# Kernel optimization log

Hardware: AMD Instinct MI355X
Metric: run time of the kernel (lower is better)

## Reference

```python
import jax, jax.numpy as jnp
import numpy as np

B, N, D_MODEL, H = 2, 2048, 1024, 16
Q_CHUNK, K_CHUNK = 512, 1024
LN_EPS = 1e-5


def layer_norm(x, g, b):
    mu = x.mean(-1, keepdims=True)
    var = ((x - mu) ** 2).mean(-1, keepdims=True)
    return (x - mu) * jax.lax.rsqrt(var + LN_EPS) * g + b


def chunked_attention(q, k, v, qry_chunk, key_chunk):
    # q,k,v: [b,h,n,d]; memory-efficient chunked online-softmax attention
    b, h, n, d = q.shape
    q = q * (d ** -0.5)
    Q, K = n // qry_chunk, n // key_chunk
    qr = q.reshape(b, h, Q, qry_chunk, d)
    kr = k.reshape(b, h, K, key_chunk, d)
    vr = v.reshape(b, h, K, key_chunk, d)
    # per (q-chunk, k-chunk) scores: [b,h,Q,K,i,j]
    qk = jnp.einsum('bhqid,bhkjd->bhqkij', qr, kr)
    qk_max = jax.lax.stop_gradient(qk.max(axis=-1, keepdims=True))  # [b,h,Q,K,i,1]
    exp_qk = jnp.exp(qk - qk_max)
    attn = jnp.einsum('bhqkij,bhkjd->bhqkid', exp_qk, vr)
    exp_sum = exp_qk.sum(-1)            # [b,h,Q,K,i]
    m = qk_max[..., 0]                  # [b,h,Q,K,i]
    gmax = m.max(axis=3, keepdims=True)  # global max over key chunks
    renorm = jax.lax.stop_gradient(jnp.exp(m - gmax))
    num = (attn * renorm[..., None]).sum(axis=3)       # [b,h,Q,i,d]
    den = (exp_sum * renorm).sum(axis=3)[..., None]    # [b,h,Q,i,1]
    out = num / (1e-8 + den)
    return out.reshape(b, h, n, d)


def setup_inputs() -> dict:
    key = jax.random.key(0)
    ks = jax.random.split(key, 10)
    s = 0.02
    return {
        'x': jax.random.normal(ks[0], (B, N, D_MODEL), dtype=jnp.float32),
        'Wq': jax.random.normal(ks[1], (D_MODEL, D_MODEL), dtype=jnp.float32) * s,
        'bq': jnp.zeros((D_MODEL,), jnp.float32),
        'Wk': jax.random.normal(ks[2], (D_MODEL, D_MODEL), dtype=jnp.float32) * s,
        'bk': jnp.zeros((D_MODEL,), jnp.float32),
        'Wv': jax.random.normal(ks[3], (D_MODEL, D_MODEL), dtype=jnp.float32) * s,
        'bv': jnp.zeros((D_MODEL,), jnp.float32),
        'Wo': jax.random.normal(ks[4], (D_MODEL, D_MODEL), dtype=jnp.float32) * s,
        'bo': jnp.zeros((D_MODEL,), jnp.float32),
        'ln_g': jnp.ones((D_MODEL,), jnp.float32),
        'ln_b': jnp.zeros((D_MODEL,), jnp.float32),
    }


def reference(x, Wq, bq, Wk, bk, Wv, bv, Wo, bo, ln_g, ln_b):
    # qkv adapter: self-attention (key = val = qry = x)
    q = x @ Wq + bq
    k = x @ Wk + bk
    v = x @ Wv + bv
    # pre-norm on query path
    q = layer_norm(q, ln_g, ln_b)
    b, n, _ = q.shape
    d = D_MODEL // H
    qh = q.reshape(b, n, H, d).transpose(0, 2, 1, 3)
    kh = k.reshape(b, n, H, d).transpose(0, 2, 1, 3)
    vh = v.reshape(b, n, H, d).transpose(0, 2, 1, 3)
    attn = chunked_attention(qh, kh, vh, Q_CHUNK, K_CHUNK)
    out = attn.transpose(0, 2, 1, 3).reshape(b, n, D_MODEL)
    out = out + q  # residual with normed projected query
    return out @ Wo + bo
```

## Files before the change

kernel.cpp:

```cpp
#include <hip/hip_runtime.h>


typedef unsigned short u16;
typedef __attribute__((ext_vector_type(8))) short bf8v;
typedef __attribute__((ext_vector_type(4))) float f4v;

typedef __attribute__((address_space(1))) void gvoid;
typedef __attribute__((address_space(3))) void lvoid;
__device__ __forceinline__ void cp16(const void* g, void* l) {
  __builtin_amdgcn_global_load_lds((gvoid*)g, (lvoid*)l, 16, 0, 0);
}

__device__ __forceinline__ float bf2f(u16 u) {
  unsigned int x = ((unsigned int)u) << 16;
  float f; __builtin_memcpy(&f, &x, 4); return f;
}
__device__ __forceinline__ u16 f2bf(float f) {
  unsigned int x; __builtin_memcpy(&x, &f, 4);
  unsigned int r = (x + 0x7fffu + ((x >> 16) & 1u)) >> 16;
  return (u16)r;
}
__device__ __forceinline__ unsigned pack2bf(float a, float b) {
  unsigned ua, ub;
  __builtin_memcpy(&ua, &a, 4); __builtin_memcpy(&ub, &b, 4);
  return __builtin_amdgcn_perm(ub, ua, 0x07060302u);
}

#define KSCALE 0.18033688011f

__global__ void k_classify(const u16* a0, const u16* a1, const u16* a2, const u16* a3,
                           const u16* a4, const u16* a5, const u16* a6, const u16* a7,
                           const u16* a8, const u16* a9, const u16* a10, int* flags) {
  int t = threadIdx.x;
  if (t >= 11) return;
  const u16* arr[11] = {a0,a1,a2,a3,a4,a5,a6,a7,a8,a9,a10};
  const u16* p = arr[t];
  int ze = 0, no = 0, pe = 0;
  for (int i = 0; i < 128; ++i) {
    u16 he = p[2*i], ho = p[2*i+1];
    if (he == 0) ze++;
    if (ho != 0) no++;
    int e = (he >> 7) & 0xff;
    if (he == 0 || (e >= 64 && e <= 160)) pe++;
  }
  int isbf;
  if (ze >= 100 && no >= 64) isbf = 0;
  else isbf = (pe >= 100) ? 1 : 0;
  flags[t] = isbf;
}

__global__ __launch_bounds__(256) void k_convert_x(const void* xin, u16* xb, const int* flags) {
  size_t i = ((size_t)blockIdx.x * 256 + threadIdx.x) * 8;
  if (flags[0]) {
    *(float4*)(xb + i) = *((const float4*)((const u16*)xin + i));
  } else {
    const float* xf = (const float*)xin;
    float4 a = *(const float4*)(xf + i);
    float4 b = *(const float4*)(xf + i + 4);
    ushort4 o0, o1;
    o0.x = f2bf(a.x); o0.y = f2bf(a.y); o0.z = f2bf(a.z); o0.w = f2bf(a.w);
    o1.x = f2bf(b.x); o1.y = f2bf(b.y); o1.z = f2bf(b.z); o1.w = f2bf(b.w);
    *(ushort4*)(xb + i) = o0; *(ushort4*)(xb + i + 4) = o1;
  }
}

__global__ __launch_bounds__(256) void k_transpose_w(const void* W0, const void* W1,
    const void* W2, const void* W3, u16* wt, const int* flags) {
  __shared__ u16 tile[64 * 65];
  int z = blockIdx.z;
  const void* W = (z == 0) ? W0 : (z == 1) ? W1 : (z == 2) ? W2 : W3;
  int isb = flags[1 + 2*z];
  u16* dst = wt + (size_t)z * (1u << 20);
  int r0 = blockIdx.y * 64, c0 = blockIdx.x * 64;
  int t = threadIdx.x;
  for (int rr = 0; rr < 2; ++rr) {
    int row = rr * 32 + (t >> 3);
    int c8 = (t & 7) * 8;
    u16 v[8];
    if (isb) {
      const u16* Ws = (const u16*)W;
      ushort4 a = *(const ushort4*)&Ws[(size_t)(r0 + row) * 1024 + c0 + c8];
      ushort4 b = *(const ushort4*)&Ws[(size_t)(r0 + row) * 1024 + c0 + c8 + 4];
      v[0]=a.x; v[1]=a.y; v[2]=a.z; v[3]=a.w; v[4]=b.x; v[5]=b.y; v[6]=b.z; v[7]=b.w;
    } else {
      const float* Wf = (const float*)W;
      float4 a = *(const float4*)&Wf[(size_t)(r0 + row) * 1024 + c0 + c8];
      float4 b = *(const float4*)&Wf[(size_t)(r0 + row) * 1024 + c0 + c8 + 4];
      v[0]=f2bf(a.x); v[1]=f2bf(a.y); v[2]=f2bf(a.z); v[3]=f2bf(a.w);
      v[4]=f2bf(b.x); v[5]=f2bf(b.y); v[6]=f2bf(b.z); v[7]=f2bf(b.w);
    }
#pragma unroll
    for (int j = 0; j < 8; ++j) tile[row * 65 + c8 + j] = v[j];
  }
  __syncthreads();
  for (int rr = 0; rr < 2; ++rr) {
    int nrow = rr * 32 + (t >> 3);
    int k8 = (t & 7) * 8;
    u16 v[8];
#pragma unroll
    for (int j = 0; j < 8; ++j) v[j] = tile[(k8 + j) * 65 + nrow];
    ushort4 o0, o1;
    o0.x=v[0]; o0.y=v[1]; o0.z=v[2]; o0.w=v[3];
    o1.x=v[4]; o1.y=v[5]; o1.z=v[6]; o1.w=v[7];
    *(ushort4*)&dst[(size_t)(c0 + nrow) * 1024 + r0 + k8] = o0;
    *(ushort4*)&dst[(size_t)(c0 + nrow) * 1024 + r0 + k8 + 4] = o1;
  }
}

template <int MT>
__device__ __forceinline__ void gemm_bt(const u16* __restrict__ A, const u16* __restrict__ Bt,
    const void* __restrict__ bias, int bias_bf, void* __restrict__ Cout, int mode,
    float cscale) {
  constexpr int MI = MT / 32;
  __shared__ __align__(16) u16 As[2][MT * 32];
  __shared__ __align__(16) u16 Bs[2][128 * 32];
  const int tid = threadIdx.x;
  const int wave = tid >> 6, lane = tid & 63;
  const int qd = lane >> 4, ln = lane & 15;
  const int m0 = blockIdx.y * MT, n0 = blockIdx.x * 128;
  const int wr = (wave >> 1) * (MT / 2), wc = (wave & 1) * 64;
  const int r0 = wave * 16 + (lane >> 2);
  const int csrc = ((lane & 3) ^ ((lane >> 2) & 3)) * 8;
  const u16* Ag = &A[(size_t)m0 * 1024];
  const u16* Bg = &Bt[(size_t)n0 * 1024];
  const int co = (qd ^ (ln & 3)) * 8;
  f4v acc[MI][4];
#pragma unroll
  for (int i = 0; i < MI; ++i)
#pragma unroll
    for (int j = 0; j < 4; ++j) acc[i][j] = (f4v){0.f, 0.f, 0.f, 0.f};

#pragma unroll
  for (int t = 0; t < MT / 64; ++t)
    cp16(&Ag[(size_t)(t * 64 + r0) * 1024 + csrc], &As[0][(t * 256 + wave * 64) * 8]);
#pragma unroll
  for (int t = 0; t < 2; ++t)
    cp16(&Bg[(size_t)(t * 64 + r0) * 1024 + csrc], &Bs[0][(t * 256 + wave * 64) * 8]);

  for (int it = 0; it < 32; ++it) {
    __syncthreads();
    if (it < 31) {
      int ko = (it + 1) * 32;
      int bi = (it + 1) & 1;
#pragma unroll
      for (int t = 0; t < MT / 64; ++t)
        cp16(&Ag[(size_t)(t * 64 + r0) * 1024 + ko + csrc], &As[bi][(t * 256 + wave * 64) * 8]);
#pragma unroll
      for (int t = 0; t < 2; ++t)
        cp16(&Bg[(size_t)(t * 64 + r0) * 1024 + ko + csrc], &Bs[bi][(t * 256 + wave * 64) * 8]);
    }
    const u16* as = As[it & 1];
    const u16* bs = Bs[it & 1];
    bf8v af[MI], bfr[4];
#pragma unroll
    for (int i = 0; i < MI; ++i) af[i]  = *(const bf8v*)&as[(wr + i * 16 + ln) * 32 + co];
#pragma unroll
    for (int j = 0; j < 4; ++j) bfr[j] = *(const bf8v*)&bs[(wc + j * 16 + ln) * 32 + co];
#pragma unroll
    for (int i = 0; i < MI; ++i)
#pragma unroll
      for (int j = 0; j < 4; ++j)
        acc[i][j] = __builtin_amdgcn_mfma_f32_16x16x32_bf16(af[i], bfr[j], acc[i][j], 0, 0, 0);
  }
#pragma unroll
  for (int j = 0; j < 4; ++j) {
    int col = n0 + wc + j * 16 + ln;
    float bv = bias_bf ? bf2f(((const u16*)bias)[col]) : ((const float*)bias)[col];
#pragma unroll
    for (int i = 0; i < MI; ++i) {
      int row = m0 + wr + i * 16 + qd * 4;
      if (mode == 2) {
        ushort4 o4;
        o4.x = f2bf((acc[i][j][0] + bv) * cscale);
        o4.y = f2bf((acc[i][j][1] + bv) * cscale);
        o4.z = f2bf((acc[i][j][2] + bv) * cscale);
        o4.w = f2bf((acc[i][j][3] + bv) * cscale);
        int b_ = row >> 11, nl = row & 2047;
        int h_ = col >> 6, d6 = col & 63;
        int kt = nl >> 6, b0 = nl & 63;
        int c = b0 >> 5, g = (b0 >> 4) & 1, qd_f = (b0 >> 2) & 3;
        int dt = d6 >> 4, ln_f = d6 & 15;
        size_t off = (size_t)(b_ * 16 + h_) * 131072
                   + (size_t)(kt * 4096 + (c * 4 + dt) * 512 + (qd_f * 16 + ln_f) * 8 + g * 4);
        *(ushort4*)&((u16*)Cout)[off] = o4;
      } else {
#pragma unroll
        for (int r = 0; r < 4; ++r) {
          float v = (acc[i][j][r] + bv) * cscale;
          if (mode == 1) ((u16*)Cout)[(size_t)(row + r) * 1024 + col] = f2bf(v);
          else           ((float*)Cout)[(size_t)(row + r) * 1024 + col] = v;
        }
      }
    }
  }
}

__global__ __launch_bounds__(256) void k_gemm_qkv(const u16* xb, const u16* wt,
    const void* bq, const void* bk, const void* bv, const int* flags,
    u16* qpre, u16* kb, u16* vtb) {
  int z = blockIdx.z;
  const u16* Bt = wt + (size_t)z * (1u << 20);
  const void* bias = (z == 0) ? bq : (z == 1) ? bk : bv;
  if (z == 0)      gemm_bt<128>(xb, Bt, bias, flags[2], qpre, 1, 1.0f);
  else if (z == 1) gemm_bt<128>(xb, Bt, bias, flags[4], kb,   1, KSCALE);
  else             gemm_bt<128>(xb, Bt, bias, flags[6], vtb,  2, 1.0f);
}

__global__ __launch_bounds__(256) void k_gemm_out(const u16* A, const u16* Bt,
    const void* bias, const int* flags, void* out) {
  gemm_bt<64>(A, Bt, bias, flags[8], out, flags[0] ? 1 : 0, 1.0f);
}

__global__ __launch_bounds__(256) void k_layernorm(const u16* __restrict__ qp,
    const void* __restrict__ g, const void* __restrict__ bb, const int* flags,
    u16* __restrict__ out) {
  int row = blockIdx.x, t = threadIdx.x;
  const u16* rp = qp + (size_t)row * 1024;
  ushort4 u = *(const ushort4*)(rp + t * 4);
  float x0 = bf2f(u.x), x1 = bf2f(u.y), x2 = bf2f(u.z), x3 = bf2f(u.w);
  float s = x0 + x1 + x2 + x3;
  float s2 = x0 * x0 + x1 * x1 + x2 * x2 + x3 * x3;
  for (int off = 32; off; off >>= 1) { s += __shfl_down(s, off); s2 += __shfl_down(s2, off); }
  __shared__ float red[10];
  int wave = t >> 6, lane = t & 63;
  if (lane == 0) { red[wave] = s; red[4 + wave] = s2; }
  __syncthreads();
  if (t == 0) {
    float S = red[0] + red[1] + red[2] + red[3];
    float S2 = red[4] + red[5] + red[6] + red[7];
    float mu = S * (1.f / 1024.f);
    float var = S2 * (1.f / 1024.f) - mu * mu;
    red[8] = mu; red[9] = rsqrtf(var + 1e-5f);
  }
  __syncthreads();
  float mu = red[8], rstd = red[9];
  int gf = flags[9], bf = flags[10];
  int c = t * 4;
  float gv[4], bv[4];
#pragma unroll
  for (int k = 0; k < 4; ++k) {
    gv[k] = gf ? bf2f(((const u16*)g)[c + k]) : ((const float*)g)[c + k];
    bv[k] = bf ? bf2f(((const u16*)bb)[c + k]) : ((const float*)bb)[c + k];
  }
  ushort4 o;
  o.x = f2bf((x0 - mu) * rstd * gv[0] + bv[0]);
  o.y = f2bf((x1 - mu) * rstd * gv[1] + bv[1]);
  o.z = f2bf((x2 - mu) * rstd * gv[2] + bv[2]);
  o.w = f2bf((x3 - mu) * rstd * gv[3] + bv[3]);
  *(ushort4*)(out + (size_t)row * 1024 + c) = o;
}

__global__ __launch_bounds__(256) void k_attention(const u16* __restrict__ qln,
    const u16* __restrict__ kb, const u16* __restrict__ vfg, u16* __restrict__ attn) {
  const int x = blockIdx.x;
  const int xcd = x & 7, sl = x >> 3;
  const int bh = xcd * 4 + (sl >> 3), qc = sl & 7;
  const int b = bh >> 4, h = bh & 15;
  const int tid = threadIdx.x, wave = tid >> 6, lane = tid & 63;
  const int qd = lane >> 4, ln = lane & 15;
  const int qrow0 = qc * 256 + wave * 64;

  const u16* kgb = kb + (size_t)b * 2048 * 1024 + h * 64;
  const u16* vgb = vfg + (size_t)bh * 131072;

  bf8v qf[4][2];
#pragma unroll
  for (int qs = 0; qs < 4; ++qs) {
    const u16* qb = qln + ((size_t)b * 2048 + qrow0 + qs * 16 + ln) * 1024 + h * 64;
    qf[qs][0] = *(const bf8v*)(qb + qd * 8);
    qf[qs][1] = *(const bf8v*)(qb + 32 + qd * 8);
  }
  float ls[4][4];
  f4v o[4][4];
#pragma unroll
  for (int qs = 0; qs < 4; ++qs)
#pragma unroll
    for (int r = 0; r < 4; ++r) { ls[qs][r] = 0.f; o[qs][r] = (f4v){0.f, 0.f, 0.f, 0.f}; }

  for (int kt = 0; kt < 2048; kt += 64) {
    const u16* kr = kgb + (size_t)kt * 1024;
    bf8v kf[4][2];
#pragma unroll
    for (int ct = 0; ct < 4; ++ct) {
      kf[ct][0] = *(const bf8v*)(kr + (size_t)(ct * 16 + ln) * 1024 + qd * 8);
      kf[ct][1] = *(const bf8v*)(kr + (size_t)(ct * 16 + ln) * 1024 + 32 + qd * 8);
    }
    const u16* vr = vgb + (size_t)(kt >> 6) * 4096;
    bf8v vf[8];
#pragma unroll
    for (int cd = 0; cd < 8; ++cd)
      vf[cd] = *(const bf8v*)(vr + cd * 512 + lane * 8);

#pragma unroll
    for (int qs = 0; qs < 4; ++qs) {
      unsigned pk[4][2];
#pragma unroll
      for (int ct = 0; ct < 4; ++ct) {
        f4v z = (f4v){0.f, 0.f, 0.f, 0.f};
        z = __builtin_amdgcn_mfma_f32_16x16x32_bf16(kf[ct][0], qf[qs][0], z, 0, 0, 0);
        z = __builtin_amdgcn_mfma_f32_16x16x32_bf16(kf[ct][1], qf[qs][1], z, 0, 0, 0);
        float p0 = __builtin_amdgcn_exp2f(z[0]);
        float p1 = __builtin_amdgcn_exp2f(z[1]);
        float p2 = __builtin_amdgcn_exp2f(z[2]);
        float p3 = __builtin_amdgcn_exp2f(z[3]);
        ls[qs][0] += p0; ls[qs][1] += p1; ls[qs][2] += p2; ls[qs][3] += p3;
        pk[ct][0] = pack2bf(p0, p1);
        pk[ct][1] = pack2bf(p2, p3);
      }
#pragma unroll
      for (int c = 0; c < 2; ++c) {
        unsigned avals[4] = {pk[2*c][0], pk[2*c][1], pk[2*c+1][0], pk[2*c+1][1]};
        bf8v af; __builtin_memcpy(&af, avals, 16);
#pragma unroll
        for (int dt = 0; dt < 4; ++dt)
          o[qs][dt] = __builtin_amdgcn_mfma_f32_16x16x32_bf16(af, vf[c * 4 + dt], o[qs][dt], 0, 0, 0);
      }
    }
  }
#pragma unroll
  for (int qs = 0; qs < 4; ++qs) {
    float lsum = (ls[qs][0] + ls[qs][1]) + (ls[qs][2] + ls[qs][3]);
    lsum += __shfl_xor(lsum, 16);
    lsum += __shfl_xor(lsum, 32);
    float rden[4];
#pragma unroll
    for (int r = 0; r < 4; ++r) {
      float dv = __shfl(lsum, (lane & 48) + qd * 4 + r);
      rden[r] = __builtin_amdgcn_rcpf(1e-8f + dv);
    }
#pragma unroll
    for (int dt = 0; dt < 4; ++dt) {
#pragma unroll
      for (int r = 0; r < 4; ++r) {
        size_t idx = ((size_t)b * 2048 + qrow0 + qs * 16 + qd * 4 + r) * 1024
                   + h * 64 + dt * 16 + ln;
        float val = o[qs][dt][r] * rden[r] + bf2f(qln[idx]);
        attn[idx] = f2bf(val);
      }
    }
  }
}

extern "C" void kernel_launch(void* const* d_in, const int* in_sizes, int n_in,
                              void* d_out, int out_size, void* d_ws, size_t ws_size,
                              hipStream_t stream) {
  int* flags = (int*)d_ws;
  u16* base = (u16*)((char*)d_ws + 256);
  const size_t M1 = 1u << 20;
  u16* xb   = base;
  u16* wt   = base + 4 * M1;
  u16* qpre = base + 8 * M1;
  u16* kb   = base + 12 * M1;
  u16* vtb  = base + 16 * M1;
  u16* qln = xb;
  u16* at  = qpre;

  k_classify<<<1, 64, 0, stream>>>(
      (const u16*)d_in[0], (const u16*)d_in[1], (const u16*)d_in[2], (const u16*)d_in[3],
      (const u16*)d_in[4], (const u16*)d_in[5], (const u16*)d_in[6], (const u16*)d_in[7],
      (const u16*)d_in[8], (const u16*)d_in[9], (const u16*)d_in[10], flags);

  k_convert_x<<<2048, 256, 0, stream>>>(d_in[0], xb, flags);
  k_transpose_w<<<dim3(16, 16, 4), 256, 0, stream>>>(d_in[1], d_in[3], d_in[5], d_in[7], wt, flags);
  k_gemm_qkv<<<dim3(8, 32, 3), 256, 0, stream>>>(xb, wt, d_in[2], d_in[4], d_in[6], flags,
                                                 qpre, kb, vtb);
  k_layernorm<<<4096, 256, 0, stream>>>(qpre, d_in[9], d_in[10], flags, qln);
  k_attention<<<256, 256, 0, stream>>>(qln, kb, vtb, at);
  k_gemm_out<<<dim3(8, 64), 256, 0, stream>>>(at, wt + 3 * M1, d_in[8], flags, d_out);
}
```

Before: 228.0 us.

## Double-buffer K loads in attention, fuse prep kernels, parallelize classify

The attention loop now uses two K fragment register buffers, so the next tile's K loads are issued before the current tile's MFMAs, letting global-load latency overlap compute. The x conversion and the weight transposes are merged into one launch to save a kernel launch and fill the GPU better. The dtype classifier now uses one wavefront per input with a shuffle reduction instead of a serial loop per thread. These changes add register pressure in attention, which could lower occupancy.

```diff
diff --git a/kernel.cpp b/kernel.cpp
--- a/kernel.cpp
+++ b/kernel.cpp
@@ -31,79 +31,87 @@
 __global__ void k_classify(const u16* a0, const u16* a1, const u16* a2, const u16* a3,
                            const u16* a4, const u16* a5, const u16* a6, const u16* a7,
                            const u16* a8, const u16* a9, const u16* a10, int* flags) {
-  int t = threadIdx.x;
-  if (t >= 11) return;
+  int w = threadIdx.x >> 6, lane = threadIdx.x & 63;
+  if (w >= 11) return;
   const u16* arr[11] = {a0,a1,a2,a3,a4,a5,a6,a7,a8,a9,a10};
-  const u16* p = arr[t];
+  const u16* p = arr[w];
   int ze = 0, no = 0, pe = 0;
-  for (int i = 0; i < 128; ++i) {
+#pragma unroll
+  for (int rep = 0; rep < 2; ++rep) {
+    int i = rep * 64 + lane;
     u16 he = p[2*i], ho = p[2*i+1];
-    if (he == 0) ze++;
-    if (ho != 0) no++;
+    ze += (he == 0);
+    no += (ho != 0);
     int e = (he >> 7) & 0xff;
-    if (he == 0 || (e >= 64 && e <= 160)) pe++;
-  }
-  int isbf;
-  if (ze >= 100 && no >= 64) isbf = 0;
-  else isbf = (pe >= 100) ? 1 : 0;
-  flags[t] = isbf;
-}
-
-__global__ __launch_bounds__(256) void k_convert_x(const void* xin, u16* xb, const int* flags) {
-  size_t i = ((size_t)blockIdx.x * 256 + threadIdx.x) * 8;
-  if (flags[0]) {
-    *(float4*)(xb + i) = *((const float4*)((const u16*)xin + i));
+    pe += (he == 0 || (e >= 64 && e <= 160));
+  }
+  for (int off = 32; off; off >>= 1) {
+    ze += __shfl_down(ze, off); no += __shfl_down(no, off); pe += __shfl_down(pe, off);
+  }
+  if (lane == 0) {
+    int isbf;
+    if (ze >= 100 && no >= 64) isbf = 0;
+    else isbf = (pe >= 100) ? 1 : 0;
+    flags[w] = isbf;
+  }
+}
+
+__global__ __launch_bounds__(256) void k_prep(const void* xin, const void* W0,
+    const void* W1, const void* W2, const void* W3, u16* xb, u16* wt, const int* flags) {
+  __shared__ u16 tile[64 * 65];
+  int bx = blockIdx.x;
+  if (bx < 1024) {
+    int z = bx >> 8, t8 = bx & 255;
+    const void* W = (z == 0) ? W0 : (z == 1) ? W1 : (z == 2) ? W2 : W3;
+    int isb = flags[1 + 2*z];
+    u16* dst = wt + (size_t)z * (1u << 20);
+    int r0 = (t8 >> 4) * 64, c0 = (t8 & 15) * 64;
+    int t = threadIdx.x;
+    for (int rr = 0; rr < 2; ++rr) {
+      int row = rr * 32 + (t >> 3);
+      int c8 = (t & 7) * 8;
+      u16 v[8];
+      if (isb) {
+        const u16* Ws = (const u16*)W;
+        ushort4 a = *(const ushort4*)&Ws[(size_t)(r0 + row) * 1024 + c0 + c8];
+        ushort4 b = *(const ushort4*)&Ws[(size_t)(r0 + row) * 1024 + c0 + c8 + 4];
+        v[0]=a.x; v[1]=a.y; v[2]=a.z; v[3]=a.w; v[4]=b.x; v[5]=b.y; v[6]=b.z; v[7]=b.w;
+      } else {
+        const float* Wf = (const float*)W;
+        float4 a = *(const float4*)&Wf[(size_t)(r0 + row) * 1024 + c0 + c8];
+        float4 b = *(const float4*)&Wf[(size_t)(r0 + row) * 1024 + c0 + c8 + 4];
+        v[0]=f2bf(a.x); v[1]=f2bf(a.y); v[2]=f2bf(a.z); v[3]=f2bf(a.w);
+        v[4]=f2bf(b.x); v[5]=f2bf(b.y); v[6]=f2bf(b.z); v[7]=f2bf(b.w);
+      }
+#pragma unroll
+      for (int j = 0; j < 8; ++j) tile[row * 65 + c8 + j] = v[j];
+    }
+    __syncthreads();
+    for (int rr = 0; rr < 2; ++rr) {
+      int nrow = rr * 32 + (t >> 3);
+      int k8 = (t & 7) * 8;
+      u16 v[8];
+#pragma unroll
+      for (int j = 0; j < 8; ++j) v[j] = tile[(k8 + j) * 65 + nrow];
+      ushort4 o0, o1;
+      o0.x=v[0]; o0.y=v[1]; o0.z=v[2]; o0.w=v[3];
+      o1.x=v[4]; o1.y=v[5]; o1.z=v[6]; o1.w=v[7];
+      *(ushort4*)&dst[(size_t)(c0 + nrow) * 1024 + r0 + k8] = o0;
+      *(ushort4*)&dst[(size_t)(c0 + nrow) * 1024 + r0 + k8 + 4] = o1;
+    }
   } else {
-    const float* xf = (const float*)xin;
-    float4 a = *(const float4*)(xf + i);
-    float4 b = *(const float4*)(xf + i + 4);
-    ushort4 o0, o1;
-    o0.x = f2bf(a.x); o0.y = f2bf(a.y); o0.z = f2bf(a.z); o0.w = f2bf(a.w);
-    o1.x = f2bf(b.x); o1.y = f2bf(b.y); o1.z = f2bf(b.z); o1.w = f2bf(b.w);
-    *(ushort4*)(xb + i) = o0; *(ushort4*)(xb + i + 4) = o1;
-  }
-}
-
-__global__ __launch_bounds__(256) void k_transpose_w(const void* W0, const void* W1,
-    const void* W2, const void* W3, u16* wt, const int* flags) {
-  __shared__ u16 tile[64 * 65];
-  int z = blockIdx.z;
-  const void* W = (z == 0) ? W0 : (z == 1) ? W1 : (z == 2) ? W2 : W3;
-  int isb = flags[1 + 2*z];
-  u16* dst = wt + (size_t)z * (1u << 20);
-  int r0 = blockIdx.y * 64, c0 = blockIdx.x * 64;
-  int t = threadIdx.x;
-  for (int rr = 0; rr < 2; ++rr) {
-    int row = rr * 32 + (t >> 3);
-    int c8 = (t & 7) * 8;
-    u16 v[8];
-    if (isb) {
-      const u16* Ws = (const u16*)W;
-      ushort4 a = *(const ushort4*)&Ws[(size_t)(r0 + row) * 1024 + c0 + c8];
-      ushort4 b = *(const ushort4*)&Ws[(size_t)(r0 + row) * 1024 + c0 + c8 + 4];
-      v[0]=a.x; v[1]=a.y; v[2]=a.z; v[3]=a.w; v[4]=b.x; v[5]=b.y; v[6]=b.z; v[7]=b.w;
+    size_t i = ((size_t)(bx - 1024) * 256 + threadIdx.x) * 8;
+    if (flags[0]) {
+      *(float4*)(xb + i) = *((const float4*)((const u16*)xin + i));
     } else {
-      const float* Wf = (const float*)W;
-      float4 a = *(const float4*)&Wf[(size_t)(r0 + row) * 1024 + c0 + c8];
-      float4 b = *(const float4*)&Wf[(size_t)(r0 + row) * 1024 + c0 + c8 + 4];
-      v[0]=f2bf(a.x); v[1]=f2bf(a.y); v[2]=f2bf(a.z); v[3]=f2bf(a.w);
-      v[4]=f2bf(b.x); v[5]=f2bf(b.y); v[6]=f2bf(b.z); v[7]=f2bf(b.w);
-    }
-#pragma unroll
-    for (int j = 0; j < 8; ++j) tile[row * 65 + c8 + j] = v[j];
-  }
-  __syncthreads();
-  for (int rr = 0; rr < 2; ++rr) {
-    int nrow = rr * 32 + (t >> 3);
-    int k8 = (t & 7) * 8;
-    u16 v[8];
-#pragma unroll
-    for (int j = 0; j < 8; ++j) v[j] = tile[(k8 + j) * 65 + nrow];
-    ushort4 o0, o1;
-    o0.x=v[0]; o0.y=v[1]; o0.z=v[2]; o0.w=v[3];
-    o1.x=v[4]; o1.y=v[5]; o1.z=v[6]; o1.w=v[7];
-    *(ushort4*)&dst[(size_t)(c0 + nrow) * 1024 + r0 + k8] = o0;
-    *(ushort4*)&dst[(size_t)(c0 + nrow) * 1024 + r0 + k8 + 4] = o1;
+      const float* xf = (const float*)xin;
+      float4 a = *(const float4*)(xf + i);
+      float4 b = *(const float4*)(xf + i + 4);
+      ushort4 o0, o1;
+      o0.x = f2bf(a.x); o0.y = f2bf(a.y); o0.z = f2bf(a.z); o0.w = f2bf(a.w);
+      o1.x = f2bf(b.x); o1.y = f2bf(b.y); o1.z = f2bf(b.z); o1.w = f2bf(b.w);
+      *(ushort4*)(xb + i) = o0; *(ushort4*)(xb + i + 4) = o1;
+    }
   }
 }
 
@@ -256,7 +264,8 @@
   const int xcd = x & 7, sl = x >> 3;
   const int bh = xcd * 4 + (sl >> 3), qc = sl & 7;
   const int b = bh >> 4, h = bh & 15;
-  const int tid = threadIdx.x, wave = tid >> 6, lane = tid & 63;
+  const int tid = threadIdx.x, lane = tid & 63;
+  const int wave = tid >> 6;
   const int qd = lane >> 4, ln = lane & 15;
   const int qrow0 = qc * 256 + wave * 64;
 
@@ -277,46 +286,66 @@
 #pragma unroll
     for (int r = 0; r < 4; ++r) { ls[qs][r] = 0.f; o[qs][r] = (f4v){0.f, 0.f, 0.f, 0.f}; }
 
-  for (int kt = 0; kt < 2048; kt += 64) {
-    const u16* kr = kgb + (size_t)kt * 1024;
-    bf8v kf[4][2];
-#pragma unroll
-    for (int ct = 0; ct < 4; ++ct) {
-      kf[ct][0] = *(const bf8v*)(kr + (size_t)(ct * 16 + ln) * 1024 + qd * 8);
-      kf[ct][1] = *(const bf8v*)(kr + (size_t)(ct * 16 + ln) * 1024 + 32 + qd * 8);
-    }
-    const u16* vr = vgb + (size_t)(kt >> 6) * 4096;
-    bf8v vf[8];
-#pragma unroll
-    for (int cd = 0; cd < 8; ++cd)
-      vf[cd] = *(const bf8v*)(vr + cd * 512 + lane * 8);
-
-#pragma unroll
-    for (int qs = 0; qs < 4; ++qs) {
-      unsigned pk[4][2];
-#pragma unroll
-      for (int ct = 0; ct < 4; ++ct) {
-        f4v z = (f4v){0.f, 0.f, 0.f, 0.f};
-        z = __builtin_amdgcn_mfma_f32_16x16x32_bf16(kf[ct][0], qf[qs][0], z, 0, 0, 0);
-        z = __builtin_amdgcn_mfma_f32_16x16x32_bf16(kf[ct][1], qf[qs][1], z, 0, 0, 0);
-        float p0 = __builtin_amdgcn_exp2f(z[0]);
-        float p1 = __builtin_amdgcn_exp2f(z[1]);
-        float p2 = __builtin_amdgcn_exp2f(z[2]);
-        float p3 = __builtin_amdgcn_exp2f(z[3]);
-        ls[qs][0] += p0; ls[qs][1] += p1; ls[qs][2] += p2; ls[qs][3] += p3;
-        pk[ct][0] = pack2bf(p0, p1);
-        pk[ct][1] = pack2bf(p2, p3);
-      }
-#pragma unroll
-      for (int c = 0; c < 2; ++c) {
-        unsigned avals[4] = {pk[2*c][0], pk[2*c][1], pk[2*c+1][0], pk[2*c+1][1]};
-        bf8v af; __builtin_memcpy(&af, avals, 16);
-#pragma unroll
-        for (int dt = 0; dt < 4; ++dt)
-          o[qs][dt] = __builtin_amdgcn_mfma_f32_16x16x32_bf16(af, vf[c * 4 + dt], o[qs][dt], 0, 0, 0);
-      }
-    }
-  }
+  bf8v kfa[4][2], kfb[4][2], vf[8];
+
+#define LOADK(kt, kf)                                                          \
+  {                                                                            \
+    const u16* kr = kgb + (size_t)(kt) * 1024;                                 \
+    _Pragma("unroll")                                                          \
+    for (int ct = 0; ct < 4; ++ct) {                                           \
+      kf[ct][0] = *(const bf8v*)(kr + (size_t)(ct * 16 + ln) * 1024 + qd * 8); \
+      kf[ct][1] = *(const bf8v*)(kr + (size_t)(ct * 16 + ln) * 1024 + 32 + qd * 8); \
+    }                                                                          \
+  }
+#define LOADV(kt)                                                              \
+  {                                                                            \
+    const u16* vr = vgb + (size_t)((kt) >> 6) * 4096;                          \
+    _Pragma("unroll")                                                          \
+    for (int cd = 0; cd < 8; ++cd)                                             \
+      vf[cd] = *(const bf8v*)(vr + cd * 512 + lane * 8);                       \
+  }
+#define COMPUTE(kf)                                                            \
+  {                                                                            \
+    _Pragma("unroll")                                                          \
+    for (int qs = 0; qs < 4; ++qs) {                                           \
+      unsigned pk[4][2];                                                       \
+      _Pragma("unroll")                                                        \
+      for (int ct = 0; ct < 4; ++ct) {                                         \
+        f4v z = (f4v){0.f, 0.f, 0.f, 0.f};                                     \
+        z = __builtin_amdgcn_mfma_f32_16x16x32_bf16(kf[ct][0], qf[qs][0], z, 0, 0, 0); \
+        z = __builtin_amdgcn_mfma_f32_16x16x32_bf16(kf[ct][1], qf[qs][1], z, 0, 0, 0); \
+        float p0 = __builtin_amdgcn_exp2f(z[0]);                               \
+        float p1 = __builtin_amdgcn_exp2f(z[1]);                               \
+        float p2 = __builtin_amdgcn_exp2f(z[2]);                               \
+        float p3 = __builtin_amdgcn_exp2f(z[3]);                               \
+        ls[qs][0] += p0; ls[qs][1] += p1; ls[qs][2] += p2; ls[qs][3] += p3;    \
+        pk[ct][0] = pack2bf(p0, p1);                                           \
+        pk[ct][1] = pack2bf(p2, p3);                                           \
+      }                                                                        \
+      _Pragma("unroll")                                                        \
+      for (int c = 0; c < 2; ++c) {                                            \
+        unsigned avals[4] = {pk[2*c][0], pk[2*c][1], pk[2*c+1][0], pk[2*c+1][1]}; \
+        bf8v af; __builtin_memcpy(&af, avals, 16);                             \
+        _Pragma("unroll")                                                      \
+        for (int dt = 0; dt < 4; ++dt)                                         \
+          o[qs][dt] = __builtin_amdgcn_mfma_f32_16x16x32_bf16(af, vf[c * 4 + dt], o[qs][dt], 0, 0, 0); \
+      }                                                                        \
+    }                                                                          \
+  }
+
+  LOADK(0, kfa);
+  for (int kt = 0; kt < 2048; kt += 128) {
+    LOADK(kt + 64, kfb);
+    LOADV(kt);
+    COMPUTE(kfa);
+    if (kt + 128 < 2048) LOADK(kt + 128, kfa);
+    LOADV(kt + 64);
+    COMPUTE(kfb);
+  }
+#undef LOADK
+#undef LOADV
+#undef COMPUTE
+
 #pragma unroll
   for (int qs = 0; qs < 4; ++qs) {
     float lsum = (ls[qs][0] + ls[qs][1]) + (ls[qs][2] + ls[qs][3]);
@@ -355,13 +384,13 @@
   u16* qln = xb;
   u16* at  = qpre;
 
-  k_classify<<<1, 64, 0, stream>>>(
+  k_classify<<<1, 704, 0, stream>>>(
       (const u16*)d_in[0], (const u16*)d_in[1], (const u16*)d_in[2], (const u16*)d_in[3],
       (const u16*)d_in[4], (const u16*)d_in[5], (const u16*)d_in[6], (const u16*)d_in[7],
       (const u16*)d_in[8], (const u16*)d_in[9], (const u16*)d_in[10], flags);
 
-  k_convert_x<<<2048, 256, 0, stream>>>(d_in[0], xb, flags);
-  k_transpose_w<<<dim3(16, 16, 4), 256, 0, stream>>>(d_in[1], d_in[3], d_in[5], d_in[7], wt, flags);
+  k_prep<<<3072, 256, 0, stream>>>(d_in[0], d_in[1], d_in[3], d_in[5], d_in[7],
+                                   xb, wt, flags);
   k_gemm_qkv<<<dim3(8, 32, 3), 256, 0, stream>>>(xb, wt, d_in[2], d_in[4], d_in[6], flags,
                                                  qpre, kb, vtb);
   k_layernorm<<<4096, 256, 0, stream>>>(qpre, d_in[9], d_in[10], flags, qln);
```

After: 229.5 us. About the same (+0.7%).
